# Optimization experiments

Measured on AMD Instinct MI355X. Metric: run time of the kernel, lower is better.

Reference implementation:

```python
import jax, jax.numpy as jnp
import numpy as np

B, N, DIM, H, DH = 8, 1024, 1024, 16, 64

def setup_inputs() -> dict:
    key = jax.random.key(0)
    ks = jax.random.split(key, 6)
    return {
        'x': jax.random.normal(ks[0], (B, N, DIM), dtype=jnp.float32),
        'freqs': jax.random.normal(ks[1], (1, N, DH), dtype=jnp.float32),
        'bias': jax.random.normal(ks[2], (1, N, DH), dtype=jnp.float32),
        'ln_gamma': jnp.ones((DIM,), jnp.float32),
        'ln_beta': jnp.zeros((DIM,), jnp.float32),
        'w_qk': jax.random.normal(ks[3], (DIM, 2 * H * DH), dtype=jnp.float32) * (DIM ** -0.5),
        'w_v': jax.random.normal(ks[4], (DIM, H * DH), dtype=jnp.float32) * (DIM ** -0.5),
        'w_out': jax.random.normal(ks[5], (H * DH, DIM), dtype=jnp.float32) * ((H * DH) ** -0.5),
        'b_out': jnp.zeros((DIM,), jnp.float32),
    }

def _apply_polar(t, freqs):
    # t: [b,h,n,d]; freqs: [1,n,d] broadcast over b,h. Output doubles last dim.
    t = jax.nn.softplus(t)
    return jnp.concatenate((t * jnp.cos(freqs), t * jnp.sin(freqs)), axis=-1)

def reference(x, freqs, bias, ln_gamma, ln_beta, w_qk, w_v, w_out, b_out):
    eps = 1e-5
    mu = jnp.mean(x, axis=-1, keepdims=True)
    var = jnp.var(x, axis=-1, keepdims=True)
    xn = (x - mu) * jax.lax.rsqrt(var + eps) * ln_gamma + ln_beta
    qk = jnp.einsum('bnd,de->bne', xn, w_qk)
    q, k = jnp.split(qk, 2, axis=-1)
    v = jnp.einsum('bnd,de->bne', xn, w_v)
    split_heads = lambda t: t.reshape(B, N, H, DH).transpose(0, 2, 1, 3)
    q, k, v = split_heads(q), split_heads(k), split_heads(v)
    q = _apply_polar(q, freqs)          # [b,h,n,2*DH]
    k = _apply_polar(k, freqs + bias)   # [b,h,n,2*DH]
    scale = DH ** -0.5
    dots = jnp.einsum('bhnd,bhmd->bhnm', q, k) * scale
    attn = jax.nn.softmax(dots, axis=-1)
    out = jnp.einsum('bhnm,bhmd->bhnd', attn, v)
    out = out.transpose(0, 2, 1, 3).reshape(B, N, H * DH)
    return jnp.einsum('bne,ed->bnd', out, w_out) + b_out
```

## Files before the change

kernel.cpp:

```cpp
#include <hip/hip_runtime.h>
#include <cmath>

using f16   = _Float16;
using f16x2 = __attribute__((ext_vector_type(2))) _Float16;
using f16x4 = __attribute__((ext_vector_type(4))) _Float16;
using f16x8 = __attribute__((ext_vector_type(8))) _Float16;
using f32x4 = __attribute__((ext_vector_type(4))) float;

#define DEV __device__ __forceinline__

constexpr int Bb  = 8;
constexpr int Nn  = 1024;
constexpr int DIM = 1024;
constexpr int Hh  = 16;
constexpr int DH  = 64;
constexpr int EQKV = 3072;

DEV void async16(const f16* g, f16* l) {
  __builtin_amdgcn_global_load_lds(
      (const __attribute__((address_space(1))) void*)g,
      (__attribute__((address_space(3))) void*)l, 16, 0, 0);
}

DEV float softplusf(float x) {
  return fmaxf(x, 0.f) + __logf(1.f + __expf(-fabsf(x)));
}

__global__ __launch_bounds__(256) void transpose_cvt3(const float* __restrict__ s0,
                                                      const float* __restrict__ s1,
                                                      const float* __restrict__ s2,
                                                      f16* __restrict__ d0,
                                                      f16* __restrict__ d2) {
  __shared__ float tile[32][33];
  const float* src; f16* dst; int cols;
  int bz = blockIdx.z;
  if (bz == 0)      { src = s0; dst = d0;                        cols = 2048; }
  else if (bz == 1) { src = s1; dst = d0 + (size_t)2048 * 1024;  cols = 1024; }
  else              { src = s2; dst = d2;                        cols = 1024; }
  int c0 = blockIdx.x * 32, r0 = blockIdx.y * 32;
  if (c0 >= cols) return;
  int t = threadIdx.x, tx = t & 31, ty = t >> 5;
#pragma unroll
  for (int j = 0; j < 32; j += 8)
    tile[ty + j][tx] = src[(size_t)(r0 + ty + j) * cols + c0 + tx];
  __syncthreads();
#pragma unroll
  for (int j = 0; j < 32; j += 8)
    dst[(size_t)(c0 + ty + j) * 1024 + r0 + tx] = (f16)tile[tx][ty + j];
}

__global__ __launch_bounds__(256) void ln_kernel(const float* __restrict__ x,
                                                 const float* __restrict__ gamma,
                                                 const float* __restrict__ beta,
                                                 f16* __restrict__ xn) {
  int row = blockIdx.x;
  int t = threadIdx.x;
  const float4* xr = (const float4*)(x + (size_t)row * DIM);
  float4 v = xr[t];
  float s  = v.x + v.y + v.z + v.w;
  float s2 = v.x * v.x + v.y * v.y + v.z * v.z + v.w * v.w;
#pragma unroll
  for (int off = 32; off; off >>= 1) {
    s  += __shfl_xor(s,  off, 64);
    s2 += __shfl_xor(s2, off, 64);
  }
  __shared__ float red[8];
  int wv = t >> 6, lane = t & 63;
  if (lane == 0) { red[wv] = s; red[4 + wv] = s2; }
  __syncthreads();
  s  = red[0] + red[1] + red[2] + red[3];
  s2 = red[4] + red[5] + red[6] + red[7];
  float mu  = s * (1.f / DIM);
  float var = s2 * (1.f / DIM) - mu * mu;
  float rs  = rsqrtf(var + 1e-5f);
  float4 g = ((const float4*)gamma)[t];
  float4 bb = ((const float4*)beta)[t];
  f16x4 o;
  o[0] = (f16)((v.x - mu) * rs * g.x + bb.x);
  o[1] = (f16)((v.y - mu) * rs * g.y + bb.y);
  o[2] = (f16)((v.z - mu) * rs * g.z + bb.z);
  o[3] = (f16)((v.w - mu) * rs * g.w + bb.w);
  ((f16x4*)(xn + (size_t)row * DIM))[t] = o;
}

template <bool FP32OUT>
__global__ __launch_bounds__(256) void gemm_bt(const f16* __restrict__ A,
                                               const f16* __restrict__ Bt,
                                               void* __restrict__ Cv,
                                               const float* __restrict__ bias,
                                               int M, int K, int E) {
  __shared__ f16 lA[128 * 32];
  __shared__ f16 lB[128 * 32];
  int tid  = threadIdx.x;
  int lane = tid & 63;
  int wv   = __builtin_amdgcn_readfirstlane(tid >> 6);
  int nbe  = E >> 7;
  int bm = blockIdx.x / nbe, be = blockIdx.x % nbe;
  size_t m0 = (size_t)bm * 128, e0 = (size_t)be * 128;
  int wm = (wv & 1) * 64, we = (wv >> 1) * 64;
  int lm = lane & 15, q = lane >> 4;

  f32x4 acc[4][4] = {};

  int row_s[2], cg_s[2];
#pragma unroll
  for (int r = 0; r < 2; ++r) {
    int s = r * 256 + tid;
    row_s[r] = s >> 2;
    cg_s[r]  = (s & 3) ^ ((row_s[r] >> 1) & 3);
  }
  const f16* pa[4];
  const f16* pb[4];
#pragma unroll
  for (int i = 0; i < 4; ++i) {
    int ra = wm + i * 16 + lm;
    pa[i] = lA + ra * 32 + (q ^ ((ra >> 1) & 3)) * 8;
    int rb = we + i * 16 + lm;
    pb[i] = lB + rb * 32 + (q ^ ((rb >> 1) & 3)) * 8;
  }

  for (int k0 = 0; k0 < K; k0 += 32) {
#pragma unroll
    for (int r = 0; r < 2; ++r) {
      const f16* ga = A  + (m0 + row_s[r]) * K + k0 + cg_s[r] * 8;
      const f16* gb = Bt + (e0 + row_s[r]) * K + k0 + cg_s[r] * 8;
      async16(ga, lA + (r * 256 + wv * 64) * 8);
      async16(gb, lB + (r * 256 + wv * 64) * 8);
    }
    __syncthreads();
    f16x8 af[4], bf[4];
#pragma unroll
    for (int i = 0; i < 4; ++i) {
      af[i] = *(const f16x8*)pa[i];
      bf[i] = *(const f16x8*)pb[i];
    }
#pragma unroll
    for (int i = 0; i < 4; ++i)
#pragma unroll
      for (int j = 0; j < 4; ++j)
        acc[i][j] = __builtin_amdgcn_mfma_f32_16x16x32_f16(af[i], bf[j], acc[i][j], 0, 0, 0);
    __syncthreads();
  }

#pragma unroll
  for (int i = 0; i < 4; ++i) {
    size_t mbase = m0 + wm + i * 16 + q * 4;
#pragma unroll
    for (int j = 0; j < 4; ++j) {
      size_t e = e0 + we + j * 16 + lm;
#pragma unroll
      for (int g = 0; g < 4; ++g) {
        float val = acc[i][j][g];
        if (FP32OUT)
          ((float*)Cv)[(mbase + g) * (size_t)E + e] = val + bias[e];
        else
          ((f16*)Cv)[(mbase + g) * (size_t)E + e] = (f16)val;
      }
    }
  }
}

template <bool FP32OUT>
__global__ __launch_bounds__(512, 2) void gemm256(const f16* __restrict__ A,
                                                  const f16* __restrict__ Bt,
                                                  void* __restrict__ Cv,
                                                  const float* __restrict__ bias,
                                                  int M, int K, int E) {
  __shared__ f16 sm[65536];
  const int tid  = threadIdx.x;
  const int lane = tid & 63;
  const int wv   = __builtin_amdgcn_readfirstlane(tid >> 6);
  const int lm   = lane & 15, q = lane >> 4;
  const int wrow = (wv >> 2) * 128;
  const int wcol = (wv & 3) * 64;

  const int nbe = E >> 8;
  const int cpx = gridDim.x >> 3;
  const int bid = blockIdx.x;
  const int swz = (bid & 7) * cpx + (bid >> 3);
  const int bm = swz / nbe, be = swz % nbe;
  const size_t m0 = (size_t)bm * 256, e0 = (size_t)be * 256;

  const int rl  = lane >> 3;
  const int pcp = lane & 7;
  const int cg  = pcp ^ rl;
  const f16* aS = A  + (m0 + (size_t)(wv * 8 + rl)) * K + cg * 8;
  const f16* bS = Bt + (e0 + (size_t)((wv >> 2) * 64 + (wv & 3) * 8 + rl)) * K + cg * 8;
  const int aDofs = wv * 512;
  const int bDofs = 16384 + ((wv >> 2) * 64 + (wv & 3) * 8) * 64;

  const int x0 = ((0 + q) ^ (lm & 7)) * 8;
  const int x1 = ((4 + q) ^ (lm & 7)) * 8;

  const int NT = K >> 6;

  async16(aS,                     sm + aDofs);
  async16(aS + (size_t)128 * K,   sm + aDofs + 128 * 64);
  async16(bS,                     sm + bDofs);
  async16(bS + (size_t)128 * K,   sm + bDofs + 128 * 64);
  async16(bS + (size_t)32 * K,    sm + bDofs + 32 * 64);
  async16(bS + (size_t)160 * K,   sm + bDofs + 160 * 64);
  async16(aS + (size_t)64 * K,    sm + aDofs + 64 * 64);
  async16(aS + (size_t)192 * K,   sm + aDofs + 192 * 64);

  f32x4 acc[8][4] = {};
  f16x8 af[4][2], bf[4][2];

  for (int t = 0; t < NT; ++t) {
    const int b = t & 1, nb = b ^ 1;
    const int tn = (t + 1 < NT) ? t + 1 : t;
    const f16* pA = sm + b * 32768;
    const f16* pB = pA + 16384;
    f16* aD = sm + nb * 32768 + aDofs;
    f16* bD = sm + nb * 32768 + bDofs;
    const f16* aSk = aS + tn * 64;
    const f16* bSk = bS + tn * 64;

    async16(aSk,                   aD);
    async16(aSk + (size_t)128 * K, aD + 128 * 64);
    asm volatile("s_waitcnt vmcnt(6)" ::: "memory");
    __builtin_amdgcn_s_barrier();
#pragma unroll
    for (int i = 0; i < 4; ++i) {
      const f16* p = pA + (wrow + i * 16 + lm) * 64;
      af[i][0] = *(const f16x8*)(p + x0);
      af[i][1] = *(const f16x8*)(p + x1);
    }
#pragma unroll
    for (int j = 0; j < 2; ++j) {
      const f16* p = pB + (wcol + j * 16 + lm) * 64;
      bf[j][0] = *(const f16x8*)(p + x0);
      bf[j][1] = *(const f16x8*)(p + x1);
    }
    __builtin_amdgcn_s_setprio(1);
#pragma unroll
    for (int i = 0; i < 4; ++i)
#pragma unroll
      for (int j = 0; j < 2; ++j) {
        acc[i][j] = __builtin_amdgcn_mfma_f32_16x16x32_f16(af[i][0], bf[j][0], acc[i][j], 0, 0, 0);
        acc[i][j] = __builtin_amdgcn_mfma_f32_16x16x32_f16(af[i][1], bf[j][1], acc[i][j], 0, 0, 0);
      }
    __builtin_amdgcn_s_setprio(0);

    async16(bSk,                   bD);
    async16(bSk + (size_t)128 * K, bD + 128 * 64);
    asm volatile("s_waitcnt vmcnt(6)" ::: "memory");
    __builtin_amdgcn_s_barrier();
#pragma unroll
    for (int j = 0; j < 2; ++j) {
      const f16* p = pB + (wcol + 32 + j * 16 + lm) * 64;
      bf[2 + j][0] = *(const f16x8*)(p + x0);
      bf[2 + j][1] = *(const f16x8*)(p + x1);
    }
    __builtin_amdgcn_s_setprio(1);
#pragma unroll
    for (int i = 0; i < 4; ++i)
#pragma unroll
      for (int j = 2; j < 4; ++j) {
        acc[i][j] = __builtin_amdgcn_mfma_f32_16x16x32_f16(af[i][0], bf[j][0], acc[i][j], 0, 0, 0);
        acc[i][j] = __builtin_amdgcn_mfma_f32_16x16x32_f16(af[i][1], bf[j][1], acc[i][j], 0, 0, 0);
      }
    __builtin_amdgcn_s_setprio(0);

    async16(bSk + (size_t)32 * K,  bD + 32 * 64);
    async16(bSk + (size_t)160 * K, bD + 160 * 64);
    async16(aSk + (size_t)64 * K,  aD + 64 * 64);
    async16(aSk + (size_t)192 * K, aD + 192 * 64);
    asm volatile("s_waitcnt vmcnt(8)" ::: "memory");
    __builtin_amdgcn_s_barrier();
#pragma unroll
    for (int i = 0; i < 4; ++i) {
      const f16* p = pA + (wrow + 64 + i * 16 + lm) * 64;
      af[i][0] = *(const f16x8*)(p + x0);
      af[i][1] = *(const f16x8*)(p + x1);
    }
    __builtin_amdgcn_s_setprio(1);
#pragma unroll
    for (int i = 0; i < 4; ++i)
#pragma unroll
      for (int j = 0; j < 4; ++j) {
        acc[4 + i][j] = __builtin_amdgcn_mfma_f32_16x16x32_f16(af[i][0], bf[j][0], acc[4 + i][j], 0, 0, 0);
        acc[4 + i][j] = __builtin_amdgcn_mfma_f32_16x16x32_f16(af[i][1], bf[j][1], acc[4 + i][j], 0, 0, 0);
      }
    __builtin_amdgcn_s_setprio(0);
  }
  asm volatile("s_waitcnt vmcnt(0)" ::: "memory");

#pragma unroll
  for (int ii = 0; ii < 8; ++ii) {
    size_t mrow = m0 + wrow + (ii >> 2) * 64 + (ii & 3) * 16 + q * 4;
#pragma unroll
    for (int j = 0; j < 4; ++j) {
      size_t e = e0 + wcol + j * 16 + lm;
#pragma unroll
      for (int g = 0; g < 4; ++g) {
        float val = acc[ii][j][g];
        if (FP32OUT)
          ((float*)Cv)[(mrow + g) * (size_t)E + e] = val + bias[e];
        else
          ((f16*)Cv)[(mrow + g) * (size_t)E + e] = (f16)val;
      }
    }
  }
}

__global__ __launch_bounds__(256) void polar_kernel(const f16* __restrict__ qkv,
                                                    const float* __restrict__ freqs,
                                                    const float* __restrict__ fbias,
                                                    f16* __restrict__ Qp,
                                                    f16* __restrict__ Kp,
                                                    f16* __restrict__ Vt) {
  __shared__ f16 vt[64 * 66];
  int tid = threadIdx.x;
  int bx = blockIdx.x;
  int nt = bx & 15, bh = bx >> 4;
  int b = bh >> 4, h = bh & 15;
  size_t tok0 = (size_t)b * Nn + nt * 64;
  int n0 = nt * 64;
  constexpr float kScale = 0.125f * 1.44269504f;
#pragma unroll
  for (int i = 0; i < 8; ++i) {
    int e2 = tid + i * 256;
    int nl = e2 >> 5, dp = (e2 & 31) * 2;
    size_t src = (tok0 + nl) * EQKV + h * 64 + dp;
    f16x2 q2 = *(const f16x2*)(qkv + src);
    f16x2 k2 = *(const f16x2*)(qkv + src + 1024);
    f16x2 v2 = *(const f16x2*)(qkv + src + 2048);
    int fidx = (n0 + nl) * 64 + dp;
    float2 f2  = *(const float2*)(freqs + fidx);
    float2 fb2 = *(const float2*)(fbias + fidx);
    f16x2 qc, qs, kc, ksn;
#pragma unroll
    for (int u = 0; u < 2; ++u) {
      float fq = u ? f2.y : f2.x;
      float fk = fq + (u ? fb2.y : fb2.x);
      float spq = softplusf((float)q2[u]) * kScale;
      float spk = softplusf((float)k2[u]);
      float snq, csq, snk, csk;
      __sincosf(fq, &snq, &csq);
      __sincosf(fk, &snk, &csk);
      qc[u]  = (f16)(spq * csq);
      qs[u]  = (f16)(spq * snq);
      kc[u]  = (f16)(spk * csk);
      ksn[u] = (f16)(spk * snk);
    }
    size_t dst = ((size_t)bh * Nn + n0 + nl) * 128 + dp;
    *(f16x2*)(Qp + dst)      = qc;
    *(f16x2*)(Qp + dst + 64) = qs;
    *(f16x2*)(Kp + dst)      = kc;
    *(f16x2*)(Kp + dst + 64) = ksn;
    vt[dp * 66 + nl]       = v2[0];
    vt[(dp + 1) * 66 + nl] = v2[1];
  }
  __syncthreads();
#pragma unroll
  for (int i = 0; i < 16; ++i) {
    int e = tid + i * 256;
    int d = e >> 6, nl = e & 63;
    Vt[((size_t)bh * 64 + d) * Nn + n0 + nl] = vt[d * 66 + nl];
  }
}

constexpr int VK0 = 0;
constexpr int VK1 = 8192;
constexpr int VV0 = 16384;
constexpr int VV1 = 21504;
constexpr int VEND = 26624;

__global__ __launch_bounds__(512, 2) void attn_kernel(const f16* __restrict__ Qp,
                                                      const f16* __restrict__ Kp,
                                                      const f16* __restrict__ Vt,
                                                      f16* __restrict__ attout) {
  __shared__ f16 smem[VEND];

  int tid = threadIdx.x, lane = tid & 63;
  int wv = __builtin_amdgcn_readfirstlane(tid >> 6);
  int lm = lane & 15, q = lane >> 4;
  int bx = blockIdx.x;
  int bh = (bx & 7) | ((bx >> 5) << 3);
  int qt = (bx >> 3) & 3;
  const f16* Kbase = Kp + (size_t)bh * Nn * 128;
  const f16* Vbase = Vt + (size_t)bh * 64 * Nn;

  {
    int idx = tid * 2;
    f16 val = (idx < 64) ? (f16)1.0f : (f16)0.0f;
    f16x2 v2i = {val, val};
    *(f16x2*)(smem + VV0 + 64 * 64 + idx) = v2i;
    *(f16x2*)(smem + VV1 + 64 * 64 + idx) = v2i;
  }

#pragma unroll
  for (int i = 0; i < 2; ++i) {
    int s = i * 512 + tid;
    int r = s >> 4, c = s & 15;
    int g = c ^ (r & 15);
    async16(Kbase + (size_t)r * 128 + g * 8, smem + VK0 + (i * 512 + wv * 64) * 8);
  }
  {
    int s = tid;
    int r = s >> 3, c = s & 7;
    int g = c ^ (r & 7);
    async16(Vbase + (size_t)r * Nn + g * 8, smem + VV0 + (wv * 64) * 8);
  }

  f16x8 qf[2][4];
  {
    const f16* Qb = Qp + ((size_t)bh * Nn + qt * 256 + wv * 32) * 128;
#pragma unroll
    for (int grp = 0; grp < 2; ++grp)
#pragma unroll
      for (int ks = 0; ks < 4; ++ks)
        qf[grp][ks] = *(const f16x8*)(Qb + (size_t)(grp * 16 + lm) * 128 + ks * 32 + q * 8);
  }

  f32x4 O[2][5] = {};
  float mrow[2] = {-INFINITY, -INFINITY};

  for (int kt = 0; kt < 16; ++kt) {
    __syncthreads();

    if (kt < 15) {
      f16* nK = smem + ((kt & 1) ? VK0 : VK1);
      f16* nV = smem + ((kt & 1) ? VV0 : VV1);
#pragma unroll
      for (int i = 0; i < 2; ++i) {
        int s = i * 512 + tid;
        int r = s >> 4, c = s & 15;
        int g = c ^ (r & 15);
        async16(Kbase + (size_t)((kt + 1) * 64 + r) * 128 + g * 8, nK + (i * 512 + wv * 64) * 8);
      }
      {
        int s = tid;
        int r = s >> 3, c = s & 7;
        int g = c ^ (r & 7);
        async16(Vbase + (size_t)r * Nn + (kt + 1) * 64 + g * 8, nV + (wv * 64) * 8);
      }
    }
    const f16* sK = smem + ((kt & 1) ? VK1 : VK0);
    const f16* sV = smem + ((kt & 1) ? VV1 : VV0);

    f32x4 S[2][4] = {};
#pragma unroll
    for (int nt = 0; nt < 4; ++nt) {
      f16x8 kf[4];
#pragma unroll
      for (int ks = 0; ks < 4; ++ks)
        kf[ks] = *(const f16x8*)(sK + (nt * 16 + lm) * 128 + (((ks * 4 + q) ^ lm) * 8));
#pragma unroll
      for (int ks = 0; ks < 4; ++ks) {
        S[0][nt] = __builtin_amdgcn_mfma_f32_16x16x32_f16(kf[ks], qf[0][ks], S[0][nt], 0, 0, 0);
        S[1][nt] = __builtin_amdgcn_mfma_f32_16x16x32_f16(kf[ks], qf[1][ks], S[1][nt], 0, 0, 0);
      }
    }

    f16x4 pf[2][4];
#pragma unroll
    for (int grp = 0; grp < 2; ++grp) {
      float mx = -INFINITY;
#pragma unroll
      for (int nt = 0; nt < 4; ++nt)
#pragma unroll
        for (int g = 0; g < 4; ++g) mx = fmaxf(mx, S[grp][nt][g]);
      mx = fmaxf(mx, __shfl_xor(mx, 16, 64));
      mx = fmaxf(mx, __shfl_xor(mx, 32, 64));
      if (!__all(mx <= mrow[grp] + 11.f)) {
        float mn = fmaxf(mrow[grp], mx);
        float alpha = __builtin_exp2f(mrow[grp] - mn);
        mrow[grp] = mn;
#pragma unroll
        for (int nto = 0; nto < 5; ++nto)
#pragma unroll
          for (int g = 0; g < 4; ++g) O[grp][nto][g] *= alpha;
      }
      float mcur = mrow[grp];
#pragma unroll
      for (int nt = 0; nt < 4; ++nt)
#pragma unroll
        for (int g = 0; g < 4; ++g)
          pf[grp][nt][g] = (f16)__builtin_exp2f(S[grp][nt][g] - mcur);
    }

#pragma unroll
    for (int nto = 0; nto < 5; ++nto) {
      int r = nto * 16 + lm;
#pragma unroll
      for (int nt = 0; nt < 4; ++nt) {
        int c16 = (nt * 2 + (q >> 1)) ^ (r & 7);
        f16x4 vf = *(const f16x4*)(sV + r * 64 + c16 * 8 + (q & 1) * 4);
        O[0][nto] = __builtin_amdgcn_mfma_f32_16x16x16f16(vf, pf[0][nt], O[0][nto], 0, 0, 0);
        O[1][nto] = __builtin_amdgcn_mfma_f32_16x16x16f16(vf, pf[1][nt], O[1][nto], 0, 0, 0);
      }
    }
  }

  int b = bh >> 4, h = bh & 15;
#pragma unroll
  for (int grp = 0; grp < 2; ++grp) {
    float l = __shfl(O[grp][4][0], lm, 64);
    float inv = 1.f / l;
    size_t token = (size_t)b * Nn + qt * 256 + wv * 32 + grp * 16 + lm;
#pragma unroll
    for (int nto = 0; nto < 4; ++nto) {
      f16x4 o4;
#pragma unroll
      for (int g = 0; g < 4; ++g) o4[g] = (f16)(O[grp][nto][g] * inv);
      *(f16x4*)(attout + token * (size_t)(Hh * DH) + h * 64 + nto * 16 + q * 4) = o4;
    }
  }
}

extern "C" void kernel_launch(void* const* d_in, const int* in_sizes, int n_in,
                              void* d_out, int out_size, void* d_ws, size_t ws_size,
                              hipStream_t stream) {
  const float* x     = (const float*)d_in[0];
  const float* freqs = (const float*)d_in[1];
  const float* fbias = (const float*)d_in[2];
  const float* gamma = (const float*)d_in[3];
  const float* beta  = (const float*)d_in[4];
  const float* w_qk  = (const float*)d_in[5];
  const float* w_v   = (const float*)d_in[6];
  const float* w_out = (const float*)d_in[7];
  const float* b_out = (const float*)d_in[8];
  float* out = (float*)d_out;

  const size_t T = (size_t)Bb * Nn;
  f16* WqkvT = (f16*)d_ws;
  f16* WoutT = WqkvT + (size_t)EQKV * DIM;
  f16* Xn    = WoutT + (size_t)DIM * DIM;
  f16* QKV   = Xn + T * DIM;
  f16* AttO  = QKV + T * EQKV;
  f16* Qp    = AttO + T * DIM;
  f16* Kp    = Qp + (size_t)128 * Nn * 128;
  f16* Vt    = Kp + (size_t)128 * Nn * 128;

  transpose_cvt3<<<dim3(64, 32, 3), 256, 0, stream>>>(w_qk, w_v, w_out, WqkvT, WoutT);

  ln_kernel<<<(int)T, 256, 0, stream>>>(x, gamma, beta, Xn);

  gemm256<false><<<(int)(T / 256) * (EQKV / 256), 512, 0, stream>>>(
      Xn, WqkvT, (void*)QKV, nullptr, (int)T, DIM, EQKV);

  polar_kernel<<<Bb * Hh * (Nn / 64), 256, 0, stream>>>(QKV, freqs, fbias, Qp, Kp, Vt);

  attn_kernel<<<Bb * Hh * (Nn / 256), 512, 0, stream>>>(Qp, Kp, Vt, AttO);

  gemm_bt<true><<<(int)(T / 128) * (DIM / 128), 256, 0, stream>>>(
      AttO, WoutT, (void*)out, b_out, (int)T, DIM, DIM);
}
```

Before: 303.7 us.

## Pipeline attention K/V loads with explicit vmcnt waits, raw barriers, and MFMA priority

```diff
diff --git a/kernel.cpp b/kernel.cpp
--- a/kernel.cpp
+++ b/kernel.cpp
@@ -389,20 +389,7 @@
     *(f16x2*)(smem + VV0 + 64 * 64 + idx) = v2i;
     *(f16x2*)(smem + VV1 + 64 * 64 + idx) = v2i;
   }
-
-#pragma unroll
-  for (int i = 0; i < 2; ++i) {
-    int s = i * 512 + tid;
-    int r = s >> 4, c = s & 15;
-    int g = c ^ (r & 15);
-    async16(Kbase + (size_t)r * 128 + g * 8, smem + VK0 + (i * 512 + wv * 64) * 8);
-  }
-  {
-    int s = tid;
-    int r = s >> 3, c = s & 7;
-    int g = c ^ (r & 7);
-    async16(Vbase + (size_t)r * Nn + g * 8, smem + VV0 + (wv * 64) * 8);
-  }
+  asm volatile("s_waitcnt lgkmcnt(0)" ::: "memory");
 
   f16x8 qf[2][4];
   {
@@ -414,33 +401,40 @@
         qf[grp][ks] = *(const f16x8*)(Qb + (size_t)(grp * 16 + lm) * 128 + ks * 32 + q * 8);
   }
 
+  const int kr0 = tid >> 4,         kc0 = tid & 15;
+  const int kg0 = kc0 ^ (kr0 & 15);
+  const int kr1 = (512 + tid) >> 4, kc1 = tid & 15;
+  const int kg1 = kc1 ^ (kr1 & 15);
+  const int vr  = tid >> 3,         vc  = tid & 7;
+  const int vg  = vc ^ (vr & 7);
+
+  async16(Kbase + (size_t)kr0 * 128 + kg0 * 8, smem + VK0 + (wv * 64) * 8);
+  async16(Kbase + (size_t)kr1 * 128 + kg1 * 8, smem + VK0 + (512 + wv * 64) * 8);
+  async16(Vbase + (size_t)vr * Nn + vg * 8,    smem + VV0 + (wv * 64) * 8);
+
   f32x4 O[2][5] = {};
   float mrow[2] = {-INFINITY, -INFINITY};
 
   for (int kt = 0; kt < 16; ++kt) {
-    __syncthreads();
-
-    if (kt < 15) {
-      f16* nK = smem + ((kt & 1) ? VK0 : VK1);
-      f16* nV = smem + ((kt & 1) ? VV0 : VV1);
-#pragma unroll
-      for (int i = 0; i < 2; ++i) {
-        int s = i * 512 + tid;
-        int r = s >> 4, c = s & 15;
-        int g = c ^ (r & 15);
-        async16(Kbase + (size_t)((kt + 1) * 64 + r) * 128 + g * 8, nK + (i * 512 + wv * 64) * 8);
-      }
-      {
-        int s = tid;
-        int r = s >> 3, c = s & 7;
-        int g = c ^ (r & 7);
-        async16(Vbase + (size_t)r * Nn + (kt + 1) * 64 + g * 8, nV + (wv * 64) * 8);
-      }
-    }
+    const int ktn = (kt < 15) ? kt + 1 : kt;
+    f16* nK = smem + ((kt & 1) ? VK0 : VK1);
+    f16* nV = smem + ((kt & 1) ? VV0 : VV1);
     const f16* sK = smem + ((kt & 1) ? VK1 : VK0);
     const f16* sV = smem + ((kt & 1) ? VV1 : VV0);
 
+    __builtin_amdgcn_s_barrier();
+
+    async16(Kbase + (size_t)(ktn * 64 + kr0) * 128 + kg0 * 8, nK + (wv * 64) * 8);
+    async16(Kbase + (size_t)(ktn * 64 + kr1) * 128 + kg1 * 8, nK + (512 + wv * 64) * 8);
+    async16(Vbase + (size_t)vr * Nn + ktn * 64 + vg * 8,      nV + (wv * 64) * 8);
+
+    asm volatile("s_waitcnt vmcnt(3)" ::: "memory");
+    __builtin_amdgcn_sched_barrier(0);
+    __builtin_amdgcn_s_barrier();
+    __builtin_amdgcn_sched_barrier(0);
+
     f32x4 S[2][4] = {};
+    __builtin_amdgcn_s_setprio(1);
 #pragma unroll
     for (int nt = 0; nt < 4; ++nt) {
       f16x8 kf[4];
@@ -453,6 +447,7 @@
         S[1][nt] = __builtin_amdgcn_mfma_f32_16x16x32_f16(kf[ks], qf[1][ks], S[1][nt], 0, 0, 0);
       }
     }
+    __builtin_amdgcn_s_setprio(0);
 
     f16x4 pf[2][4];
 #pragma unroll
@@ -481,6 +476,7 @@
           pf[grp][nt][g] = (f16)__builtin_exp2f(S[grp][nt][g] - mcur);
     }
 
+    __builtin_amdgcn_s_setprio(1);
 #pragma unroll
     for (int nto = 0; nto < 5; ++nto) {
       int r = nto * 16 + lm;
@@ -492,7 +488,9 @@
         O[1][nto] = __builtin_amdgcn_mfma_f32_16x16x16f16(vf, pf[1][nt], O[1][nto], 0, 0, 0);
       }
     }
-  }
+    __builtin_amdgcn_s_setprio(0);
+  }
+  asm volatile("s_waitcnt vmcnt(0)" ::: "memory");
 
   int b = bh >> 4, h = bh & 15;
 #pragma unroll
```

New measurement: 325.3 us. 1.07x slower.
